# Kernel tuning notes

Measured on AMD Instinct MI355X. Metric: run time of the kernel, lower is better.

Reference implementation:

```python
import jax, jax.numpy as jnp
import numpy as np

B, S, ENC = 16, 1500, 1280      # batch, audio frames, encoder dim
K = 2                            # pool stride -> in_dim = ENC*K
IN_DIM = ENC * K                 # 2560
LLM = 2048                       # output dim
HID = 512                        # expert hidden dim
E, TOPK = 8, 2                   # num experts, top-k
EPS = 1e-6


def _ln(x, g, b):
    m = jnp.mean(x, -1, keepdims=True)
    v = jnp.mean((x - m) ** 2, -1, keepdims=True)
    return (x - m) * jax.lax.rsqrt(v + EPS) * g + b


def _swiglu(x, w12, w3):
    # w12: [2H, D], w3: [O, H]; dropout is identity at inference
    h = x @ w12.T
    gate, val = jnp.split(h, 2, axis=-1)
    return (jax.nn.silu(gate) * val) @ w3.T


def setup_inputs() -> dict:
    key = jax.random.key(0)
    ks = jax.random.split(key, 12)
    sc = 0.02
    return {
        "x": jax.random.normal(ks[0], (B, S, ENC), jnp.float32),
        "ln_pre_g": 1.0 + sc * jax.random.normal(ks[1], (IN_DIM,), jnp.float32),
        "ln_pre_b": sc * jax.random.normal(ks[2], (IN_DIM,), jnp.float32),
        "router_w": sc * jax.random.normal(ks[3], (E, IN_DIM), jnp.float32),
        "router_b": sc * jax.random.normal(ks[4], (E,), jnp.float32),
        "shared_w12": sc * jax.random.normal(ks[5], (2 * HID, IN_DIM), jnp.float32),
        "shared_w3": sc * jax.random.normal(ks[6], (LLM, HID), jnp.float32),
        "experts_w12": sc * jax.random.normal(ks[7], (E, 2 * HID, IN_DIM), jnp.float32),
        "experts_w3": sc * jax.random.normal(ks[8], (E, LLM, HID), jnp.float32),
        "ln_post_g": 1.0 + sc * jax.random.normal(ks[9], (LLM,), jnp.float32),
        "ln_post_b": sc * jax.random.normal(ks[10], (LLM,), jnp.float32),
    }


def reference(x, ln_pre_g, ln_pre_b, router_w, router_b,
              shared_w12, shared_w3, experts_w12, experts_w3,
              ln_post_g, ln_post_b):
    b, s, d = x.shape
    pad = (-s) % K
    if pad:
        x = jnp.pad(x, ((0, 0), (0, pad), (0, 0)))
    xk = x.reshape(b, -1, d * K)          # [B, S/K, IN_DIM]
    new_s = xk.shape[1]
    nx = _ln(xk.reshape(-1, d * K), ln_pre_g, ln_pre_b)   # [T, IN_DIM]

    shared = _swiglu(nx, shared_w12, shared_w3)            # [T, LLM]

    logits = nx @ router_w.T + router_b                    # [T, E]
    probs = jax.nn.softmax(logits, -1)
    w, idx = jax.lax.top_k(probs, TOPK)                    # [T, K]
    w = w / (jnp.sum(w, -1, keepdims=True) + 1e-20)
    # combine[t, e] = sum_k w[t,k] * (idx[t,k]==e)  (equiv to masked loop + scatter-add)
    combine = jnp.sum(jax.nn.one_hot(idx, E, dtype=nx.dtype) * w[..., None], axis=1)  # [T, E]

    hid = jnp.einsum('td,efd->tef', nx, experts_w12)       # [T, E, 2H]
    gate, val = jnp.split(hid, 2, axis=-1)
    act = jax.nn.silu(gate) * val                          # [T, E, H]
    eo = jnp.einsum('teh,eoh->teo', act, experts_w3)       # [T, E, LLM]
    routed = jnp.einsum('teo,te->to', eo, combine)         # [T, LLM]

    out = _ln(shared + routed, ln_post_g, ln_post_b)
    return out.reshape(b, new_s, LLM)
```

## Files before the change

### kernel.cpp

```cpp
#include <hip/hip_runtime.h>

#define T_TOK 12000
#define NSLOT 24000
#define DIN 2560
#define DH 512
#define DOUT 2048
#define NEXP 8
#define MSH 12000
#define SHBASE 24000

typedef unsigned short u16;
typedef unsigned int u32;
typedef __attribute__((ext_vector_type(4))) float f32x4;
typedef __attribute__((ext_vector_type(8))) short short8;
typedef __attribute__((ext_vector_type(4))) u16 u16x4;
typedef __attribute__((ext_vector_type(8))) u16 u16x8;

__device__ __forceinline__ u16 f2bf(float f) {
  u32 u = __builtin_bit_cast(u32, f);
  return (u16)((u + 0x7fffu + ((u >> 16) & 1u)) >> 16);
}
__device__ __forceinline__ float bf2f(u16 h) {
  return __builtin_bit_cast(float, (u32)h << 16);
}

__device__ __forceinline__ void gload_lds16(const void* g, void* l) {
  __builtin_amdgcn_global_load_lds((const __attribute__((address_space(1))) u32*)g,
                                   (__attribute__((address_space(3))) u32*)l, 16, 0, 0);
}

__global__ __launch_bounds__(256) void cvt_bf16_kernel(const float* __restrict__ in,
                                                       u16* __restrict__ out, int n4) {
  const int i = blockIdx.x * 256 + threadIdx.x;
  if (i >= n4) return;
  f32x4 v = ((const f32x4*)in)[i];
  u16x4 o = { f2bf(v.x), f2bf(v.y), f2bf(v.z), f2bf(v.w) };
  ((u16x4*)out)[i] = o;
}

__global__ __launch_bounds__(256) void ln_router_kernel(
    const float* __restrict__ x, const float* __restrict__ gamma, const float* __restrict__ beta,
    const float* __restrict__ rw, const float* __restrict__ rb,
    u16* __restrict__ nx, int* __restrict__ tok_e, float* __restrict__ tok_w,
    int* __restrict__ count) {
  const int t = blockIdx.x * 4 + (threadIdx.x >> 6);
  const int lane = threadIdx.x & 63;
  const f32x4* xrow = (const f32x4*)(x + (size_t)t * DIN);

  f32x4 xv[10];
  float s = 0.f, s2 = 0.f;
#pragma unroll
  for (int c = 0; c < 10; ++c) {
    xv[c] = xrow[c * 64 + lane];
#pragma unroll
    for (int i = 0; i < 4; ++i) { s += xv[c][i]; s2 += xv[c][i] * xv[c][i]; }
  }
#pragma unroll
  for (int off = 32; off > 0; off >>= 1) {
    s += __shfl_xor(s, off);
    s2 += __shfl_xor(s2, off);
  }
  const float mean = s * (1.0f / DIN);
  const float var = s2 * (1.0f / DIN) - mean * mean;
  const float rstd = rsqrtf(var + 1e-6f);

  u16* nxrow = nx + (size_t)t * DIN;
#pragma unroll
  for (int c = 0; c < 10; ++c) {
    f32x4 g = ((const f32x4*)gamma)[c * 64 + lane];
    f32x4 b = ((const f32x4*)beta)[c * 64 + lane];
    xv[c] = (xv[c] - mean) * rstd * g + b;
    u16x4 p = { f2bf(xv[c].x), f2bf(xv[c].y), f2bf(xv[c].z), f2bf(xv[c].w) };
    ((u16x4*)nxrow)[c * 64 + lane] = p;
  }

  float lp[NEXP];
#pragma unroll
  for (int e = 0; e < NEXP; ++e) {
    const f32x4* rwe = (const f32x4*)(rw + (size_t)e * DIN);
    float acc = 0.f;
#pragma unroll
    for (int c = 0; c < 10; ++c) {
      f32x4 r = rwe[c * 64 + lane];
      acc += xv[c].x * r.x + xv[c].y * r.y + xv[c].z * r.z + xv[c].w * r.w;
    }
    lp[e] = acc;
  }
#pragma unroll
  for (int e = 0; e < NEXP; ++e)
#pragma unroll
    for (int off = 32; off > 0; off >>= 1) lp[e] += __shfl_xor(lp[e], off);

  if (lane == 0) {
    float lg[NEXP];
#pragma unroll
    for (int e = 0; e < NEXP; ++e) lg[e] = lp[e] + rb[e];
    float mx = lg[0];
#pragma unroll
    for (int e = 1; e < NEXP; ++e) mx = fmaxf(mx, lg[e]);
    float p[NEXP], ps = 0.f;
#pragma unroll
    for (int e = 0; e < NEXP; ++e) { p[e] = expf(lg[e] - mx); ps += p[e]; }
    int i0 = 0;
#pragma unroll
    for (int e = 1; e < NEXP; ++e) if (p[e] > p[i0]) i0 = e;
    int i1 = (i0 == 0) ? 1 : 0;
#pragma unroll
    for (int e = 0; e < NEXP; ++e) if (e != i0 && p[e] > p[i1]) i1 = e;
    float w0 = p[i0] / ps, w1 = p[i1] / ps;
    const float inv = 1.0f / (w0 + w1 + 1e-20f);
    w0 *= inv; w1 *= inv;
    tok_e[2 * t] = i0; tok_e[2 * t + 1] = i1;
    tok_w[2 * t] = w0; tok_w[2 * t + 1] = w1;
    atomicAdd(&count[i0 * 32], 1);
    atomicAdd(&count[i1 * 32], 1);
  }
}

__global__ void prefix_kernel(const int* __restrict__ count, int* __restrict__ prefix) {
  if (threadIdx.x == 0) {
    int acc = 0;
    for (int e = 0; e < NEXP; ++e) { prefix[e] = acc; acc += count[e * 32]; }
  }
}

__global__ __launch_bounds__(256) void assign_kernel(
    const int* __restrict__ tok_e, const float* __restrict__ tok_w, const int* __restrict__ prefix,
    int* __restrict__ cursor, int* __restrict__ slot_token, float* __restrict__ slot_w,
    int* __restrict__ token_slot) {
  const int t = blockIdx.x * 256 + threadIdx.x;
  if (t >= T_TOK) return;
#pragma unroll
  for (int k = 0; k < 2; ++k) {
    const int e = tok_e[2 * t + k];
    const int pos = atomicAdd(&cursor[e * 32], 1);
    const int sl = prefix[e] + pos;
    slot_token[sl] = t;
    slot_w[sl] = tok_w[2 * t + k];
    token_slot[2 * t + k] = sl;
  }
}

template <int PHASE>
__global__ __launch_bounds__(256, 2) void gemm_moe(
    const u16* __restrict__ A0, const u16* __restrict__ Bsh, const u16* __restrict__ Bex,
    u16* __restrict__ C,
    const int* __restrict__ cnt32, const int* __restrict__ prefix,
    const int* __restrict__ slot_token, const float* __restrict__ slot_w) {
  constexpr int N = (PHASE == 1) ? 1024 : 2048;
  constexpr int K = (PHASE == 1) ? 2560 : 512;
  constexpr int NX = N / 128;

  __shared__ u16 ldsA[128 * 64];
  __shared__ u16 ldsB[128 * 64];

  int A_act = 0;
#pragma unroll
  for (int ee = 0; ee < 9; ++ee) {
    const int c = (ee == 8) ? MSH : cnt32[ee * 32];
    A_act += ((c + 127) >> 7) * NX;
  }
  const int bid = blockIdx.x;
  if (bid >= A_act) return;

  const int xcd = bid & 7, rank = bid >> 3;
  const int q = A_act >> 3, r = A_act & 7;
  const int tile = (xcd < r ? xcd * (q + 1) : r * (q + 1) + (xcd - r) * q) + rank;

  int e = 8, local = 0, m_valid = MSH, row_off = 0;
  {
    int bacc = 0, found = 0;
#pragma unroll
    for (int ee = 0; ee < 9; ++ee) {
      const int c = (ee == 8) ? MSH : cnt32[ee * 32];
      const int w = ((c + 127) >> 7) * NX;
      if (!found && tile < bacc + w) {
        found = 1; e = ee; local = tile - bacc; m_valid = c;
        row_off = (ee == 8) ? 0 : prefix[ee];
      }
      bacc += w;
    }
  }
  const int ty = local / NX;
  const int tx = local % NX;
  const int crow_base = (e == 8) ? SHBASE : row_off;
  const u16* Bb = (e == 8) ? Bsh : Bex + (size_t)e * N * K;

  const int tid = threadIdx.x;
  const int lane = tid & 63;
  const int wid = tid >> 6;
  const int sk8 = ((lane & 7) ^ (lane >> 3)) * 8;

  const u16* aptr[4];
  const u16* bptr[4];
#pragma unroll
  for (int i = 0; i < 4; ++i) {
    const int rr = wid * 32 + i * 8 + (lane >> 3);
    int gr = ty * 128 + rr;
    gr = gr < m_valid ? gr : (m_valid - 1);
    int ar;
    if constexpr (PHASE == 1) ar = (e == 8) ? gr : slot_token[row_off + gr];
    else                      ar = crow_base + gr;
    aptr[i] = A0 + (size_t)ar * K;
    bptr[i] = Bb + (size_t)(tx * 128 + rr) * K;
  }

  const f32x4 zero = {0.f, 0.f, 0.f, 0.f};
  f32x4 acc[4][4];
#pragma unroll
  for (int m = 0; m < 4; ++m)
#pragma unroll
    for (int n = 0; n < 4; ++n) acc[m][n] = zero;

  const int wr = (wid >> 1) * 64;
  const int wc = (wid & 1) * 64;
  const int fr = lane & 15;
  const int fk = (lane >> 4) * 8;

  for (int k0 = 0; k0 < K; k0 += 64) {
#pragma unroll
    for (int i = 0; i < 4; ++i) {
      gload_lds16(aptr[i] + k0 + sk8, &ldsA[(wid * 4 + i) * 512]);
      gload_lds16(bptr[i] + k0 + sk8, &ldsB[(wid * 4 + i) * 512]);
    }
    __syncthreads();
#pragma unroll
    for (int kk = 0; kk < 2; ++kk) {
      short8 af[4], bfm[4];
      const int kbs = (kk * 32 + fk) ^ ((lane & 7) << 3);
#pragma unroll
      for (int m = 0; m < 4; ++m)
        af[m] = *(const short8*)&ldsA[(wr + m * 16 + fr) * 64 + kbs];
#pragma unroll
      for (int n = 0; n < 4; ++n)
        bfm[n] = *(const short8*)&ldsB[(wc + n * 16 + fr) * 64 + kbs];
#pragma unroll
      for (int m = 0; m < 4; ++m)
#pragma unroll
        for (int n = 0; n < 4; ++n)
          acc[m][n] = __builtin_amdgcn_mfma_f32_16x16x32_bf16(af[m], bfm[n], acc[m][n], 0, 0, 0);
    }
    __syncthreads();
  }

  const int ccol = wc + (lane & 15);
#pragma unroll
  for (int m = 0; m < 4; ++m) {
#pragma unroll
    for (int i = 0; i < 4; ++i) {
      const int row = wr + m * 16 + (lane >> 4) * 4 + i;
      const int gr = ty * 128 + row;
      if (gr < m_valid) {
        float wscale = 1.0f;
        if constexpr (PHASE == 2) wscale = (e == 8) ? 1.0f : slot_w[row_off + gr];
        u16* crow = C + (size_t)(crow_base + gr) * N + tx * 128;
#pragma unroll
        for (int n = 0; n < 4; ++n) crow[ccol + n * 16] = f2bf(acc[m][n][i] * wscale);
      }
    }
  }
}

__global__ __launch_bounds__(256) void act_kernel(const u16* __restrict__ h,
                                                  u16* __restrict__ a, int rows) {
  const int idx = blockIdx.x * 256 + threadIdx.x;
  if (idx >= rows * 64) return;
  const int r = idx >> 6;
  const int c = (idx & 63) * 8;
  u16x8 g8 = *(const u16x8*)&h[(size_t)r * 1024 + c];
  u16x8 v8 = *(const u16x8*)&h[(size_t)r * 1024 + 512 + c];
  u16x8 o;
#pragma unroll
  for (int i = 0; i < 8; ++i) {
    const float g = bf2f(g8[i]);
    const float v = bf2f(v8[i]);
    const float sig = 1.0f / (1.0f + __expf(-g));
    o[i] = f2bf(g * sig * v);
  }
  *(u16x8*)&a[(size_t)r * 512 + c] = o;
}

__global__ __launch_bounds__(256) void final_ln_kernel(
    const u16* __restrict__ O16, const int* __restrict__ token_slot,
    const float* __restrict__ gamma, const float* __restrict__ beta, float* __restrict__ out) {
  const int t = blockIdx.x;
  const int tid = threadIdx.x;
  const int lane = tid & 63;
  const int wv = tid >> 6;
  const int s0 = token_slot[2 * t], s1 = token_slot[2 * t + 1];
  const int c = tid * 8;
  u16x8 a8 = *(const u16x8*)&O16[(size_t)(SHBASE + t) * DOUT + c];
  u16x8 b8 = *(const u16x8*)&O16[(size_t)s0 * DOUT + c];
  u16x8 c8 = *(const u16x8*)&O16[(size_t)s1 * DOUT + c];
  float v[8];
  float s = 0.f, s2 = 0.f;
#pragma unroll
  for (int i = 0; i < 8; ++i) {
    v[i] = bf2f(a8[i]) + bf2f(b8[i]) + bf2f(c8[i]);
    s += v[i];
    s2 += v[i] * v[i];
  }
#pragma unroll
  for (int off = 32; off > 0; off >>= 1) {
    s += __shfl_xor(s, off);
    s2 += __shfl_xor(s2, off);
  }
  __shared__ float red[4][2];
  if (lane == 0) { red[wv][0] = s; red[wv][1] = s2; }
  __syncthreads();
  const float S = red[0][0] + red[1][0] + red[2][0] + red[3][0];
  const float S2 = red[0][1] + red[1][1] + red[2][1] + red[3][1];
  const float mean = S * (1.0f / DOUT);
  const float var = S2 * (1.0f / DOUT) - mean * mean;
  const float rstd = rsqrtf(var + 1e-6f);
  f32x4 g0 = ((const f32x4*)gamma)[tid * 2], g1 = ((const f32x4*)gamma)[tid * 2 + 1];
  f32x4 be0 = ((const f32x4*)beta)[tid * 2], be1 = ((const f32x4*)beta)[tid * 2 + 1];
  f32x4 o0, o1;
#pragma unroll
  for (int i = 0; i < 4; ++i) {
    o0[i] = (v[i] - mean) * rstd * g0[i] + be0[i];
    o1[i] = (v[4 + i] - mean) * rstd * g1[i] + be1[i];
  }
  f32x4* orow = (f32x4*)(out + (size_t)t * DOUT);
  orow[tid * 2] = o0;
  orow[tid * 2 + 1] = o1;
}

extern "C" void kernel_launch(void* const* d_in, const int* in_sizes, int n_in,
                              void* d_out, int out_size, void* d_ws, size_t ws_size,
                              hipStream_t stream) {
  (void)in_sizes; (void)n_in; (void)out_size; (void)ws_size;
  const float* x = (const float*)d_in[0];
  const float* ln_pre_g = (const float*)d_in[1];
  const float* ln_pre_b = (const float*)d_in[2];
  const float* router_w = (const float*)d_in[3];
  const float* router_b = (const float*)d_in[4];
  const float* shared_w12 = (const float*)d_in[5];
  const float* shared_w3 = (const float*)d_in[6];
  const float* experts_w12 = (const float*)d_in[7];
  const float* experts_w3 = (const float*)d_in[8];
  const float* ln_post_g = (const float*)d_in[9];
  const float* ln_post_b = (const float*)d_in[10];
  float* out = (float*)d_out;

  size_t off = 0;
  char* ws = (char*)d_ws;
  auto take = [&](size_t bytes) -> void* {
    void* p = ws + off;
    off += (bytes + 255) & ~(size_t)255;
    return p;
  };
  u16* w12s = (u16*)take((size_t)1024 * 2560 * 2);
  u16* w3s  = (u16*)take((size_t)2048 * 512 * 2);
  u16* ew12 = (u16*)take((size_t)NEXP * 1024 * 2560 * 2);
  u16* ew3  = (u16*)take((size_t)NEXP * 2048 * 512 * 2);
  u16* nx   = (u16*)take((size_t)T_TOK * DIN * 2);
  u16* act  = (u16*)take((size_t)36000 * DH * 2);
  u16* O16  = (u16*)take((size_t)36000 * DOUT * 2);
  u16* H    = O16;
  int* tok_e = (int*)take(NSLOT * 4);
  float* tok_w = (float*)take(NSLOT * 4);
  int* slot_token = (int*)take(NSLOT * 4);
  float* slot_w = (float*)take(NSLOT * 4);
  int* token_slot = (int*)take(NSLOT * 4);
  int* cnt = (int*)take(3 * 8 * 32 * 4);
  int* cursor = cnt + 8 * 32;
  int* prefix = cnt + 2 * 8 * 32;

  hipMemsetAsync(cnt, 0, 3 * 8 * 32 * 4, stream);

  cvt_bf16_kernel<<<(1024 * 2560 / 4 + 255) / 256, 256, 0, stream>>>(shared_w12, w12s, 1024 * 2560 / 4);
  cvt_bf16_kernel<<<(2048 * 512 / 4 + 255) / 256, 256, 0, stream>>>(shared_w3, w3s, 2048 * 512 / 4);
  cvt_bf16_kernel<<<(NEXP * 1024 * 2560 / 4 + 255) / 256, 256, 0, stream>>>(experts_w12, ew12, NEXP * 1024 * 2560 / 4);
  cvt_bf16_kernel<<<(NEXP * 2048 * 512 / 4 + 255) / 256, 256, 0, stream>>>(experts_w3, ew3, NEXP * 2048 * 512 / 4);

  ln_router_kernel<<<T_TOK / 4, 256, 0, stream>>>(x, ln_pre_g, ln_pre_b, router_w, router_b,
                                                  nx, tok_e, tok_w, cnt);
  prefix_kernel<<<1, 64, 0, stream>>>(cnt, prefix);
  assign_kernel<<<(T_TOK + 255) / 256, 256, 0, stream>>>(tok_e, tok_w, prefix, cursor,
                                                         slot_token, slot_w, token_slot);

  gemm_moe<1><<<(187 + 8 + 94) * 8, 256, 0, stream>>>(nx, w12s, ew12, H,
                                                      cnt, prefix, slot_token, slot_w);
  act_kernel<<<36000 * 64 / 256, 256, 0, stream>>>(H, act, 36000);
  gemm_moe<2><<<(187 + 8 + 94) * 16, 256, 0, stream>>>(act, w3s, ew3, O16,
                                                       cnt, prefix, slot_token, slot_w);

  final_ln_kernel<<<T_TOK, 256, 0, stream>>>(O16, token_slot, ln_post_g, ln_post_b, out);
}
```

Baseline: 607.2 us.

## Enlarge MoE GEMM tiles to 256x256 with double-buffered LDS prefetch

The grouped MoE GEMM moves from 128x128 tiles with 256 threads to 256x256 tiles with 512 threads (8 waves, each computing a 128x64 sub-tile). A/B tiles are double-buffered in LDS: the next k-slice is loaded asynchronously while the current one is consumed, with explicit vmcnt waits and barriers replacing the two syncthreads per iteration. B fragments are held in registers across the M loop, and MFMA bursts are wrapped in raised wave priority. This aims for more data reuse per global load and better overlap of memory and compute. The cost is 128KB of LDS per block, so only one block fits per CU, and far fewer tiles, which raises tail and load-imbalance risk.

```diff
diff --git a/kernel.cpp b/kernel.cpp
--- a/kernel.cpp
+++ b/kernel.cpp
@@ -142,23 +142,24 @@
 }
 
 template <int PHASE>
-__global__ __launch_bounds__(256, 2) void gemm_moe(
+__global__ __launch_bounds__(512, 1) void gemm_moe(
     const u16* __restrict__ A0, const u16* __restrict__ Bsh, const u16* __restrict__ Bex,
     u16* __restrict__ C,
     const int* __restrict__ cnt32, const int* __restrict__ prefix,
     const int* __restrict__ slot_token, const float* __restrict__ slot_w) {
   constexpr int N = (PHASE == 1) ? 1024 : 2048;
   constexpr int K = (PHASE == 1) ? 2560 : 512;
-  constexpr int NX = N / 128;
-
-  __shared__ u16 ldsA[128 * 64];
-  __shared__ u16 ldsB[128 * 64];
+  constexpr int NXT = N / 256;
+  constexpr int NK = K / 64;
+
+  __shared__ u16 ldsA[2][256 * 64];
+  __shared__ u16 ldsB[2][256 * 64];
 
   int A_act = 0;
 #pragma unroll
   for (int ee = 0; ee < 9; ++ee) {
     const int c = (ee == 8) ? MSH : cnt32[ee * 32];
-    A_act += ((c + 127) >> 7) * NX;
+    A_act += ((c + 255) >> 8) * NXT;
   }
   const int bid = blockIdx.x;
   if (bid >= A_act) return;
@@ -173,7 +174,7 @@
 #pragma unroll
     for (int ee = 0; ee < 9; ++ee) {
       const int c = (ee == 8) ? MSH : cnt32[ee * 32];
-      const int w = ((c + 127) >> 7) * NX;
+      const int w = ((c + 255) >> 8) * NXT;
       if (!found && tile < bacc + w) {
         found = 1; e = ee; local = tile - bacc; m_valid = c;
         row_off = (ee == 8) ? 0 : prefix[ee];
@@ -181,81 +182,116 @@
       bacc += w;
     }
   }
-  const int ty = local / NX;
-  const int tx = local % NX;
+  const int ty = local / NXT;
+  const int tx = local % NXT;
   const int crow_base = (e == 8) ? SHBASE : row_off;
   const u16* Bb = (e == 8) ? Bsh : Bex + (size_t)e * N * K;
 
   const int tid = threadIdx.x;
   const int lane = tid & 63;
   const int wid = tid >> 6;
-  const int sk8 = ((lane & 7) ^ (lane >> 3)) * 8;
-
+  const int wm = wid >> 2;
+  const int wn = wid & 3;
+
+  const int srow = tid >> 3;
+  const int sk8e = ((tid & 7) ^ (srow & 7)) * 8;
   const u16* aptr[4];
   const u16* bptr[4];
 #pragma unroll
-  for (int i = 0; i < 4; ++i) {
-    const int rr = wid * 32 + i * 8 + (lane >> 3);
-    int gr = ty * 128 + rr;
+  for (int j = 0; j < 4; ++j) {
+    int gr = ty * 256 + j * 64 + srow;
     gr = gr < m_valid ? gr : (m_valid - 1);
     int ar;
     if constexpr (PHASE == 1) ar = (e == 8) ? gr : slot_token[row_off + gr];
     else                      ar = crow_base + gr;
-    aptr[i] = A0 + (size_t)ar * K;
-    bptr[i] = Bb + (size_t)(tx * 128 + rr) * K;
+    aptr[j] = A0 + (size_t)ar * K + sk8e;
+    bptr[j] = Bb + (size_t)(tx * 256 + j * 64 + srow) * K + sk8e;
+  }
+
+#define STAGE(buf, k0)                                                     \
+  {                                                                        \
+    _Pragma("unroll")                                                      \
+    for (int j = 0; j < 4; ++j) {                                          \
+      gload_lds16(aptr[j] + (k0), &ldsA[buf][j * 4096 + wid * 512]);       \
+      gload_lds16(bptr[j] + (k0), &ldsB[buf][j * 4096 + wid * 512]);       \
+    }                                                                      \
   }
 
   const f32x4 zero = {0.f, 0.f, 0.f, 0.f};
-  f32x4 acc[4][4];
-#pragma unroll
-  for (int m = 0; m < 4; ++m)
+  f32x4 acc[8][4];
+#pragma unroll
+  for (int m = 0; m < 8; ++m)
 #pragma unroll
     for (int n = 0; n < 4; ++n) acc[m][n] = zero;
 
-  const int wr = (wid >> 1) * 64;
-  const int wc = (wid & 1) * 64;
   const int fr = lane & 15;
   const int fk = (lane >> 4) * 8;
-
-  for (int k0 = 0; k0 < K; k0 += 64) {
+  const int sx = (lane & 7) << 3;
+
+  STAGE(0, 0);
+
+#pragma unroll 1
+  for (int kt = 0; kt < NK; ++kt) {
+    const int cur = kt & 1;
+    if (kt + 1 < NK) {
+      STAGE(cur ^ 1, (kt + 1) * 64);
+      asm volatile("s_waitcnt vmcnt(8)" ::: "memory");
+    } else {
+      asm volatile("s_waitcnt vmcnt(0)" ::: "memory");
+    }
+    __builtin_amdgcn_s_barrier();
+    __builtin_amdgcn_sched_barrier(0);
+
+    short8 bfr[4][2];
+#pragma unroll
+    for (int n = 0; n < 4; ++n)
+#pragma unroll
+      for (int kk = 0; kk < 2; ++kk) {
+        const int brow = wn * 64 + n * 16 + fr;
+        const int kc = (kk * 32 + fk) ^ sx;
+        bfr[n][kk] = *(const short8*)&ldsB[cur][brow * 64 + kc];
+      }
+#pragma unroll
+    for (int p = 0; p < 4; ++p) {
+      short8 af[2][2];
+#pragma unroll
+      for (int mi = 0; mi < 2; ++mi)
+#pragma unroll
+        for (int kk = 0; kk < 2; ++kk) {
+          const int arow = wm * 128 + (p * 2 + mi) * 16 + fr;
+          const int kc = (kk * 32 + fk) ^ sx;
+          af[mi][kk] = *(const short8*)&ldsA[cur][arow * 64 + kc];
+        }
+      __builtin_amdgcn_s_setprio(1);
+#pragma unroll
+      for (int mi = 0; mi < 2; ++mi)
+#pragma unroll
+        for (int n = 0; n < 4; ++n)
+#pragma unroll
+          for (int kk = 0; kk < 2; ++kk)
+            acc[p * 2 + mi][n] = __builtin_amdgcn_mfma_f32_16x16x32_bf16(
+                af[mi][kk], bfr[n][kk], acc[p * 2 + mi][n], 0, 0, 0);
+      __builtin_amdgcn_s_setprio(0);
+    }
+
+    __builtin_amdgcn_sched_barrier(0);
+    __builtin_amdgcn_s_barrier();
+  }
+#undef STAGE
+
+  const int ccol = tx * 256 + wn * 64 + (lane & 15);
+#pragma unroll
+  for (int m = 0; m < 8; ++m) {
 #pragma unroll
     for (int i = 0; i < 4; ++i) {
-      gload_lds16(aptr[i] + k0 + sk8, &ldsA[(wid * 4 + i) * 512]);
-      gload_lds16(bptr[i] + k0 + sk8, &ldsB[(wid * 4 + i) * 512]);
-    }
-    __syncthreads();
-#pragma unroll
-    for (int kk = 0; kk < 2; ++kk) {
-      short8 af[4], bfm[4];
-      const int kbs = (kk * 32 + fk) ^ ((lane & 7) << 3);
-#pragma unroll
-      for (int m = 0; m < 4; ++m)
-        af[m] = *(const short8*)&ldsA[(wr + m * 16 + fr) * 64 + kbs];
-#pragma unroll
-      for (int n = 0; n < 4; ++n)
-        bfm[n] = *(const short8*)&ldsB[(wc + n * 16 + fr) * 64 + kbs];
-#pragma unroll
-      for (int m = 0; m < 4; ++m)
-#pragma unroll
-        for (int n = 0; n < 4; ++n)
-          acc[m][n] = __builtin_amdgcn_mfma_f32_16x16x32_bf16(af[m], bfm[n], acc[m][n], 0, 0, 0);
-    }
-    __syncthreads();
-  }
-
-  const int ccol = wc + (lane & 15);
-#pragma unroll
-  for (int m = 0; m < 4; ++m) {
-#pragma unroll
-    for (int i = 0; i < 4; ++i) {
-      const int row = wr + m * 16 + (lane >> 4) * 4 + i;
-      const int gr = ty * 128 + row;
+      const int row = wm * 128 + m * 16 + (lane >> 4) * 4 + i;
+      const int gr = ty * 256 + row;
       if (gr < m_valid) {
         float wscale = 1.0f;
         if constexpr (PHASE == 2) wscale = (e == 8) ? 1.0f : slot_w[row_off + gr];
-        u16* crow = C + (size_t)(crow_base + gr) * N + tx * 128;
-#pragma unroll
-        for (int n = 0; n < 4; ++n) crow[ccol + n * 16] = f2bf(acc[m][n][i] * wscale);
+        u16* crow = C + (size_t)(crow_base + gr) * N + ccol;
+#pragma unroll
+        for (int n = 0; n < 4; ++n) crow[n * 16] = f2bf(acc[m][n][i] * wscale);
       }
     }
   }
@@ -380,11 +416,11 @@
   assign_kernel<<<(T_TOK + 255) / 256, 256, 0, stream>>>(tok_e, tok_w, prefix, cursor,
                                                          slot_token, slot_w, token_slot);
 
-  gemm_moe<1><<<(187 + 8 + 94) * 8, 256, 0, stream>>>(nx, w12s, ew12, H,
-                                                      cnt, prefix, slot_token, slot_w);
+  gemm_moe<1><<<148 * 4, 512, 0, stream>>>(nx, w12s, ew12, H,
+                                           cnt, prefix, slot_token, slot_w);
   act_kernel<<<36000 * 64 / 256, 256, 0, stream>>>(H, act, 36000);
-  gemm_moe<2><<<(187 + 8 + 94) * 16, 256, 0, stream>>>(act, w3s, ew3, O16,
-                                                       cnt, prefix, slot_token, slot_w);
+  gemm_moe<2><<<148 * 8, 512, 0, stream>>>(act, w3s, ew3, O16,
+                                           cnt, prefix, slot_token, slot_w);
 
   final_ln_kernel<<<T_TOK, 256, 0, stream>>>(O16, token_slot, ln_post_g, ln_post_b, out);
 }
```

New measurement: 665.4 us. 9.6% more time.

## Fuse SwiGLU activation into first expert GEMM epilogue via paired gate/value tiles

Applied to the files above, without the earlier changes.

The first GEMM now loads matching gate and value weight tiles (rows tx*128 and 512+tx*128) into separate LDS buffers and keeps two accumulator sets per block. SiLU(gate)*value is computed in the epilogue and written straight into the 512-wide activation buffer. This removes the separate activation kernel and the bf16 round-trip of the 1024-wide hidden tensor. In exchange it doubles the accumulator registers and adds 50% more LDS per block, which may lower occupancy or cause spills under the 2-blocks-per-CU launch bound.

```diff
diff --git a/kernel.cpp b/kernel.cpp
--- a/kernel.cpp
+++ b/kernel.cpp
@@ -141,18 +141,16 @@
   }
 }
 
-template <int PHASE>
-__global__ __launch_bounds__(256, 2) void gemm_moe(
+__global__ __launch_bounds__(256, 2) void gemm_ffn1(
     const u16* __restrict__ A0, const u16* __restrict__ Bsh, const u16* __restrict__ Bex,
-    u16* __restrict__ C,
+    u16* __restrict__ ACT,
     const int* __restrict__ cnt32, const int* __restrict__ prefix,
-    const int* __restrict__ slot_token, const float* __restrict__ slot_w) {
-  constexpr int N = (PHASE == 1) ? 1024 : 2048;
-  constexpr int K = (PHASE == 1) ? 2560 : 512;
-  constexpr int NX = N / 128;
-
+    const int* __restrict__ slot_token) {
+  constexpr int K = 2560;
+  constexpr int NX = 4;
   __shared__ u16 ldsA[128 * 64];
-  __shared__ u16 ldsB[128 * 64];
+  __shared__ u16 ldsG[128 * 64];
+  __shared__ u16 ldsV[128 * 64];
 
   int A_act = 0;
 #pragma unroll
@@ -184,7 +182,7 @@
   const int ty = local / NX;
   const int tx = local % NX;
   const int crow_base = (e == 8) ? SHBASE : row_off;
-  const u16* Bb = (e == 8) ? Bsh : Bex + (size_t)e * N * K;
+  const u16* Bb = (e == 8) ? Bsh : Bex + (size_t)e * 1024 * K;
 
   const int tid = threadIdx.x;
   const int lane = tid & 63;
@@ -192,25 +190,25 @@
   const int sk8 = ((lane & 7) ^ (lane >> 3)) * 8;
 
   const u16* aptr[4];
-  const u16* bptr[4];
+  const u16* gptr[4];
+  const u16* vptr[4];
 #pragma unroll
   for (int i = 0; i < 4; ++i) {
     const int rr = wid * 32 + i * 8 + (lane >> 3);
     int gr = ty * 128 + rr;
     gr = gr < m_valid ? gr : (m_valid - 1);
-    int ar;
-    if constexpr (PHASE == 1) ar = (e == 8) ? gr : slot_token[row_off + gr];
-    else                      ar = crow_base + gr;
+    const int ar = (e == 8) ? gr : slot_token[row_off + gr];
     aptr[i] = A0 + (size_t)ar * K;
-    bptr[i] = Bb + (size_t)(tx * 128 + rr) * K;
+    gptr[i] = Bb + (size_t)(tx * 128 + rr) * K;
+    vptr[i] = Bb + (size_t)(512 + tx * 128 + rr) * K;
   }
 
   const f32x4 zero = {0.f, 0.f, 0.f, 0.f};
-  f32x4 acc[4][4];
+  f32x4 accg[4][4], accv[4][4];
 #pragma unroll
   for (int m = 0; m < 4; ++m)
 #pragma unroll
-    for (int n = 0; n < 4; ++n) acc[m][n] = zero;
+    for (int n = 0; n < 4; ++n) { accg[m][n] = zero; accv[m][n] = zero; }
 
   const int wr = (wid >> 1) * 64;
   const int wc = (wid & 1) * 64;
@@ -221,24 +219,29 @@
 #pragma unroll
     for (int i = 0; i < 4; ++i) {
       gload_lds16(aptr[i] + k0 + sk8, &ldsA[(wid * 4 + i) * 512]);
-      gload_lds16(bptr[i] + k0 + sk8, &ldsB[(wid * 4 + i) * 512]);
+      gload_lds16(gptr[i] + k0 + sk8, &ldsG[(wid * 4 + i) * 512]);
+      gload_lds16(vptr[i] + k0 + sk8, &ldsV[(wid * 4 + i) * 512]);
     }
     __syncthreads();
 #pragma unroll
     for (int kk = 0; kk < 2; ++kk) {
-      short8 af[4], bfm[4];
+      short8 af[4], bg[4], bv[4];
       const int kbs = (kk * 32 + fk) ^ ((lane & 7) << 3);
 #pragma unroll
       for (int m = 0; m < 4; ++m)
         af[m] = *(const short8*)&ldsA[(wr + m * 16 + fr) * 64 + kbs];
 #pragma unroll
-      for (int n = 0; n < 4; ++n)
-        bfm[n] = *(const short8*)&ldsB[(wc + n * 16 + fr) * 64 + kbs];
+      for (int n = 0; n < 4; ++n) {
+        bg[n] = *(const short8*)&ldsG[(wc + n * 16 + fr) * 64 + kbs];
+        bv[n] = *(const short8*)&ldsV[(wc + n * 16 + fr) * 64 + kbs];
+      }
 #pragma unroll
       for (int m = 0; m < 4; ++m)
 #pragma unroll
-        for (int n = 0; n < 4; ++n)
-          acc[m][n] = __builtin_amdgcn_mfma_f32_16x16x32_bf16(af[m], bfm[n], acc[m][n], 0, 0, 0);
+        for (int n = 0; n < 4; ++n) {
+          accg[m][n] = __builtin_amdgcn_mfma_f32_16x16x32_bf16(af[m], bg[n], accg[m][n], 0, 0, 0);
+          accv[m][n] = __builtin_amdgcn_mfma_f32_16x16x32_bf16(af[m], bv[n], accv[m][n], 0, 0, 0);
+        }
     }
     __syncthreads();
   }
@@ -251,33 +254,131 @@
       const int row = wr + m * 16 + (lane >> 4) * 4 + i;
       const int gr = ty * 128 + row;
       if (gr < m_valid) {
-        float wscale = 1.0f;
-        if constexpr (PHASE == 2) wscale = (e == 8) ? 1.0f : slot_w[row_off + gr];
+        u16* crow = ACT + (size_t)(crow_base + gr) * DH + tx * 128;
+#pragma unroll
+        for (int n = 0; n < 4; ++n) {
+          const float g = accg[m][n][i];
+          const float v = accv[m][n][i];
+          const float sig = 1.0f / (1.0f + __expf(-g));
+          crow[ccol + n * 16] = f2bf(g * sig * v);
+        }
+      }
+    }
+  }
+}
+
+__global__ __launch_bounds__(256, 2) void gemm_ffn2(
+    const u16* __restrict__ A0, const u16* __restrict__ Bsh, const u16* __restrict__ Bex,
+    u16* __restrict__ C,
+    const int* __restrict__ cnt32, const int* __restrict__ prefix,
+    const float* __restrict__ slot_w) {
+  constexpr int N = 2048;
+  constexpr int K = 512;
+  constexpr int NX = 16;
+  __shared__ u16 ldsA[128 * 64];
+  __shared__ u16 ldsB[128 * 64];
+
+  int A_act = 0;
+#pragma unroll
+  for (int ee = 0; ee < 9; ++ee) {
+    const int c = (ee == 8) ? MSH : cnt32[ee * 32];
+    A_act += ((c + 127) >> 7) * NX;
+  }
+  const int bid = blockIdx.x;
+  if (bid >= A_act) return;
+
+  const int xcd = bid & 7, rank = bid >> 3;
+  const int q = A_act >> 3, r = A_act & 7;
+  const int tile = (xcd < r ? xcd * (q + 1) : r * (q + 1) + (xcd - r) * q) + rank;
+
+  int e = 8, local = 0, m_valid = MSH, row_off = 0;
+  {
+    int bacc = 0, found = 0;
+#pragma unroll
+    for (int ee = 0; ee < 9; ++ee) {
+      const int c = (ee == 8) ? MSH : cnt32[ee * 32];
+      const int w = ((c + 127) >> 7) * NX;
+      if (!found && tile < bacc + w) {
+        found = 1; e = ee; local = tile - bacc; m_valid = c;
+        row_off = (ee == 8) ? 0 : prefix[ee];
+      }
+      bacc += w;
+    }
+  }
+  const int ty = local / NX;
+  const int tx = local % NX;
+  const int crow_base = (e == 8) ? SHBASE : row_off;
+  const u16* Bb = (e == 8) ? Bsh : Bex + (size_t)e * N * K;
+
+  const int tid = threadIdx.x;
+  const int lane = tid & 63;
+  const int wid = tid >> 6;
+  const int sk8 = ((lane & 7) ^ (lane >> 3)) * 8;
+
+  const u16* aptr[4];
+  const u16* bptr[4];
+#pragma unroll
+  for (int i = 0; i < 4; ++i) {
+    const int rr = wid * 32 + i * 8 + (lane >> 3);
+    int gr = ty * 128 + rr;
+    gr = gr < m_valid ? gr : (m_valid - 1);
+    aptr[i] = A0 + (size_t)(crow_base + gr) * K;
+    bptr[i] = Bb + (size_t)(tx * 128 + rr) * K;
+  }
+
+  const f32x4 zero = {0.f, 0.f, 0.f, 0.f};
+  f32x4 acc[4][4];
+#pragma unroll
+  for (int m = 0; m < 4; ++m)
+#pragma unroll
+    for (int n = 0; n < 4; ++n) acc[m][n] = zero;
+
+  const int wr = (wid >> 1) * 64;
+  const int wc = (wid & 1) * 64;
+  const int fr = lane & 15;
+  const int fk = (lane >> 4) * 8;
+
+  for (int k0 = 0; k0 < K; k0 += 64) {
+#pragma unroll
+    for (int i = 0; i < 4; ++i) {
+      gload_lds16(aptr[i] + k0 + sk8, &ldsA[(wid * 4 + i) * 512]);
+      gload_lds16(bptr[i] + k0 + sk8, &ldsB[(wid * 4 + i) * 512]);
+    }
+    __syncthreads();
+#pragma unroll
+    for (int kk = 0; kk < 2; ++kk) {
+      short8 af[4], bfm[4];
+      const int kbs = (kk * 32 + fk) ^ ((lane & 7) << 3);
+#pragma unroll
+      for (int m = 0; m < 4; ++m)
+        af[m] = *(const short8*)&ldsA[(wr + m * 16 + fr) * 64 + kbs];
+#pragma unroll
+      for (int n = 0; n < 4; ++n)
+        bfm[n] = *(const short8*)&ldsB[(wc + n * 16 + fr) * 64 + kbs];
+#pragma unroll
+      for (int m = 0; m < 4; ++m)
+#pragma unroll
+        for (int n = 0; n < 4; ++n)
+          acc[m][n] = __builtin_amdgcn_mfma_f32_16x16x32_bf16(af[m], bfm[n], acc[m][n], 0, 0, 0);
+    }
+    __syncthreads();
+  }
+
+  const int ccol = wc + (lane & 15);
+#pragma unroll
+  for (int m = 0; m < 4; ++m) {
+#pragma unroll
+    for (int i = 0; i < 4; ++i) {
+      const int row = wr + m * 16 + (lane >> 4) * 4 + i;
+      const int gr = ty * 128 + row;
+      if (gr < m_valid) {
+        const float wscale = (e == 8) ? 1.0f : slot_w[row_off + gr];
         u16* crow = C + (size_t)(crow_base + gr) * N + tx * 128;
 #pragma unroll
         for (int n = 0; n < 4; ++n) crow[ccol + n * 16] = f2bf(acc[m][n][i] * wscale);
       }
     }
   }
-}
-
-__global__ __launch_bounds__(256) void act_kernel(const u16* __restrict__ h,
-                                                  u16* __restrict__ a, int rows) {
-  const int idx = blockIdx.x * 256 + threadIdx.x;
-  if (idx >= rows * 64) return;
-  const int r = idx >> 6;
-  const int c = (idx & 63) * 8;
-  u16x8 g8 = *(const u16x8*)&h[(size_t)r * 1024 + c];
-  u16x8 v8 = *(const u16x8*)&h[(size_t)r * 1024 + 512 + c];
-  u16x8 o;
-#pragma unroll
-  for (int i = 0; i < 8; ++i) {
-    const float g = bf2f(g8[i]);
-    const float v = bf2f(v8[i]);
-    const float sig = 1.0f / (1.0f + __expf(-g));
-    o[i] = f2bf(g * sig * v);
-  }
-  *(u16x8*)&a[(size_t)r * 512 + c] = o;
 }
 
 __global__ __launch_bounds__(256) void final_ln_kernel(
@@ -357,7 +458,6 @@
   u16* nx   = (u16*)take((size_t)T_TOK * DIN * 2);
   u16* act  = (u16*)take((size_t)36000 * DH * 2);
   u16* O16  = (u16*)take((size_t)36000 * DOUT * 2);
-  u16* H    = O16;
   int* tok_e = (int*)take(NSLOT * 4);
   float* tok_w = (float*)take(NSLOT * 4);
   int* slot_token = (int*)take(NSLOT * 4);
@@ -380,11 +480,8 @@
   assign_kernel<<<(T_TOK + 255) / 256, 256, 0, stream>>>(tok_e, tok_w, prefix, cursor,
                                                          slot_token, slot_w, token_slot);
 
-  gemm_moe<1><<<(187 + 8 + 94) * 8, 256, 0, stream>>>(nx, w12s, ew12, H,
-                                                      cnt, prefix, slot_token, slot_w);
-  act_kernel<<<36000 * 64 / 256, 256, 0, stream>>>(H, act, 36000);
-  gemm_moe<2><<<(187 + 8 + 94) * 16, 256, 0, stream>>>(act, w3s, ew3, O16,
-                                                       cnt, prefix, slot_token, slot_w);
+  gemm_ffn1<<<289 * 4, 256, 0, stream>>>(nx, w12s, ew12, act, cnt, prefix, slot_token);
+  gemm_ffn2<<<289 * 16, 256, 0, stream>>>(act, w3s, ew3, O16, cnt, prefix, slot_w);
 
   final_ln_kernel<<<T_TOK, 256, 0, stream>>>(O16, token_slot, ln_post_g, ln_post_b, out);
 }
```

Result: slower. 620.3 us (+2.2%).
